# Optimization experiments

Hardware: AMD Instinct MI355X
Metric: run time of the kernel (lower is better)

Reference implementation:

```python
import jax, jax.numpy as jnp
import numpy as np

B, N, C, H, T = 64, 4096, 768, 12, 10


def setup_inputs() -> dict:
    key = jax.random.key(0)
    kx, kq, kk, kv, kp = jax.random.split(key, 5)
    std = 0.02  # trunc_normal std from _init_weights
    return {
        "x": jax.random.normal(kx, (B, N, C), jnp.float32),
        "Wq": std * jax.random.normal(kq, (C, C), jnp.float32),
        "Wk": std * jax.random.normal(kk, (C, C), jnp.float32),
        "Wv": std * jax.random.normal(kv, (C, C), jnp.float32),
        "Wp": std * jax.random.normal(kp, (C, C), jnp.float32),
        "bp": jnp.zeros((C,), jnp.float32),
        "nb_task_tokens": T,
    }


def reference(x, Wq, Wk, Wv, Wp, bp, nb_task_tokens):
    Bq, Nq, Cq = x.shape
    d = Cq // H
    scale = d ** -0.5
    Tt = nb_task_tokens
    # q only from the first T (task) tokens; k, v from all N tokens
    q = (x[:, :Tt] @ Wq).reshape(Bq, Tt, H, d).transpose(0, 2, 1, 3) * scale  # [B,H,T,d]
    k = (x @ Wk).reshape(Bq, Nq, H, d).transpose(0, 2, 1, 3)                  # [B,H,N,d]
    v = (x @ Wv).reshape(Bq, Nq, H, d).transpose(0, 2, 1, 3)                  # [B,H,N,d]
    attn = jnp.einsum("bhtd,bhnd->bhtn", q, k)                                # [B,H,T,N]
    # mask: task token i may attend to itself and to all patch tokens (cols >= T),
    # but not to other task tokens
    rows = jnp.arange(Tt)[:, None]
    cols = jnp.arange(Nq)[None, :]
    allowed = (cols >= Tt) | (cols == rows)                                   # [T,N]
    attn = jnp.where(allowed, attn, -jnp.inf)
    attn = jax.nn.softmax(attn, axis=-1)
    x_cls = jnp.einsum("bhtn,bhnd->bhtd", attn, v)                            # [B,H,T,d]
    x_cls = x_cls.transpose(0, 2, 1, 3).reshape(Bq, Tt, Cq)
    x_cls = x_cls @ Wp + bp
    return (x_cls, attn, v)
```

## Files before the change

kernel.cpp:

```cpp
#include <hip/hip_runtime.h>

typedef __attribute__((ext_vector_type(8))) short short8;
typedef __attribute__((ext_vector_type(4))) short short4v;
typedef __attribute__((ext_vector_type(4))) float f32x4;

__device__ __forceinline__ unsigned short f2bf(float f) {
  union { float f; unsigned u; } v; v.f = f;
  unsigned r = v.u + 0x7FFFu + ((v.u >> 16) & 1u);
  return (unsigned short)(r >> 16);
}

__device__ __forceinline__ void gload16(const void* g, void* l) {
  __builtin_amdgcn_global_load_lds(
      (const __attribute__((address_space(1))) void*)g,
      (__attribute__((address_space(3))) void*)l, 16, 0, 0);
}

__global__ __launch_bounds__(256) void conv_x(const float* __restrict__ x,
                                              unsigned short* __restrict__ xb) {
  const long total = 25165824;
  long stride = (long)gridDim.x * 256;
  for (long u = blockIdx.x * 256 + threadIdx.x; u < total; u += stride) {
    const float* p = x + u * 8;
    float4 a = *(const float4*)p;
    float4 b = *(const float4*)(p + 4);
    short8 h;
    h[0] = (short)f2bf(a.x); h[1] = (short)f2bf(a.y);
    h[2] = (short)f2bf(a.z); h[3] = (short)f2bf(a.w);
    h[4] = (short)f2bf(b.x); h[5] = (short)f2bf(b.y);
    h[6] = (short)f2bf(b.z); h[7] = (short)f2bf(b.w);
    *(short8*)(xb + u * 8) = h;
  }
}

__global__ __launch_bounds__(256) void prep_w(const float* __restrict__ Wk,
                                              const float* __restrict__ Wv,
                                              unsigned short* __restrict__ Wt) {
  int idx = blockIdx.x * 256 + threadIdx.x;
  int n = idx / 768, k = idx - n * 768;
  float w = (n < 768) ? Wk[k * 768 + n] : Wv[k * 768 + (n - 768)];
  Wt[idx] = f2bf(w);
}

__global__ __launch_bounds__(256) void q_proj(const float* __restrict__ x,
                                              const float* __restrict__ Wq,
                                              unsigned short* __restrict__ q_ws) {
  int b = blockIdx.x, tid = threadIdx.x;
  __shared__ float xr[7680];
  const float* xp = x + (long)b * 4096 * 768;
  for (int i = tid; i < 7680; i += 256) xr[i] = xp[i];
  for (int i = tid; i < 12 * 6 * 64; i += 256) {
    int h = i / 384, rem = i - h * 384;
    int t = 10 + rem / 64, d = rem & 63;
    q_ws[(((long)(b * 12 + h) * 16 + t) << 6) + d] = 0;
  }
  __syncthreads();
  float acc[10][3];
#pragma unroll
  for (int t = 0; t < 10; ++t) { acc[t][0] = 0.f; acc[t][1] = 0.f; acc[t][2] = 0.f; }
  for (int k = 0; k < 768; ++k) {
    const float* wr = Wq + (long)k * 768;
    float w0 = wr[tid], w1 = wr[tid + 256], w2 = wr[tid + 512];
#pragma unroll
    for (int t = 0; t < 10; ++t) {
      float xv = xr[t * 768 + k];
      acc[t][0] += xv * w0; acc[t][1] += xv * w1; acc[t][2] += xv * w2;
    }
  }
#pragma unroll
  for (int t = 0; t < 10; ++t) {
#pragma unroll
    for (int j = 0; j < 3; ++j) {
      int c = tid + j * 256;
      int h = c >> 6, d = c & 63;
      q_ws[(((long)(b * 12 + h) * 16 + t) << 6) + d] = f2bf(acc[t][j] * 0.125f);
    }
  }
}

__global__ __launch_bounds__(256) void gemm_kv5(const unsigned short* __restrict__ xb,
                                                const unsigned short* __restrict__ Wt,
                                                unsigned short* __restrict__ k_ws,
                                                float* __restrict__ v_out) {
  __shared__ char smem[49152];
#define A0 ((unsigned short*)(smem + 0))
#define B0 ((unsigned short*)(smem + 8192))
#define A1 ((unsigned short*)(smem + 16384))
#define B1 ((unsigned short*)(smem + 24576))
#define A2 ((unsigned short*)(smem + 32768))
#define B2 ((unsigned short*)(smem + 40960))

  int bid = blockIdx.x;
  int lb = (bid & 7) * 3072 + (bid >> 3);
  int mt = lb / 12, nt = lb - mt * 12;
  long m0 = (long)mt * 128; int n0 = nt * 128;
  int tid = threadIdx.x, lane = tid & 63;
  int uw = __builtin_amdgcn_readfirstlane(tid >> 6);
  int wm = uw >> 1, wn = uw & 1;
  int r16 = lane & 15, gk = lane >> 4;

  const unsigned short* xs = xb + m0 * 768;
  const unsigned short* wp = Wt + (long)n0 * 768;

  int srow = lane >> 2;
  int sg = ((lane & 3) ^ ((srow >> 1) & 3)) << 3;
  int sw = (gk ^ ((r16 >> 1) & 3)) << 3;

  int c0 = uw, c1 = uw + 4;
  const unsigned short* pA0 = xs + (long)(c0 * 16 + srow) * 768 + sg;
  const unsigned short* pA1 = xs + (long)(c1 * 16 + srow) * 768 + sg;
  const unsigned short* pB0 = wp + (long)(c0 * 16 + srow) * 768 + sg;
  const unsigned short* pB1 = wp + (long)(c1 * 16 + srow) * 768 + sg;

  f32x4 acc[4][4];
#pragma unroll
  for (int i = 0; i < 4; ++i)
#pragma unroll
    for (int j = 0; j < 4; ++j) acc[i][j] = (f32x4){0.f, 0.f, 0.f, 0.f};

#define STAGE(Ab, Bb, OFF)                                                      \
  {                                                                             \
    gload16(pA0 + (OFF), &Ab[c0 * 512]);                                        \
    gload16(pA1 + (OFF), &Ab[c1 * 512]);                                        \
    gload16(pB0 + (OFF), &Bb[c0 * 512]);                                        \
    gload16(pB1 + (OFF), &Bb[c1 * 512]);                                        \
  }
#define COMPUTE(Ab, Bb)                                                         \
  {                                                                             \
    short8 af[4], bfr[4];                                                       \
    _Pragma("unroll")                                                           \
    for (int mi = 0; mi < 4; ++mi)                                              \
      af[mi] = *(const short8*)&Ab[(wm * 64 + mi * 16 + r16) * 32 + sw];        \
    _Pragma("unroll")                                                           \
    for (int ni = 0; ni < 4; ++ni)                                              \
      bfr[ni] = *(const short8*)&Bb[(wn * 64 + ni * 16 + r16) * 32 + sw];       \
    _Pragma("unroll")                                                           \
    for (int mi = 0; mi < 4; ++mi)                                              \
      _Pragma("unroll")                                                         \
      for (int ni = 0; ni < 4; ++ni)                                            \
        acc[mi][ni] = __builtin_amdgcn_mfma_f32_16x16x32_bf16(af[mi], bfr[ni],  \
                                                              acc[mi][ni], 0, 0, 0); \
  }
#define WB4 asm volatile("s_waitcnt vmcnt(4) lgkmcnt(0)\n\ts_barrier" ::: "memory")
#define WB0 asm volatile("s_waitcnt vmcnt(0) lgkmcnt(0)\n\ts_barrier" ::: "memory")

  STAGE(A0, B0, 0);
  STAGE(A1, B1, 32);
  WB4;

#pragma unroll 1
  for (int g = 0; g < 7; ++g) {
    STAGE(A2, B2, 64);  COMPUTE(A0, B0); WB4;
    STAGE(A0, B0, 96);  COMPUTE(A1, B1); WB4;
    STAGE(A1, B1, 128); COMPUTE(A2, B2); WB4;
    pA0 += 96; pA1 += 96; pB0 += 96; pB1 += 96;
  }
  STAGE(A2, B2, 64); COMPUTE(A0, B0); WB4;
  COMPUTE(A1, B1); WB0;
  COMPUTE(A2, B2);

#undef STAGE
#undef COMPUTE
#undef WB4
#undef WB0

  float* scr = (float*)(smem + uw * 4096);
  bool is_k = (n0 < 768);
  int cb = is_k ? n0 : n0 - 768;
  int hq = (cb >> 6) + wn;
  int b12h = 0;

#pragma unroll
  for (int mi = 0; mi < 4; ++mi) {
#pragma unroll
    for (int ni = 0; ni < 4; ++ni)
#pragma unroll
      for (int r = 0; r < 4; ++r)
        scr[(gk * 4 + r) * 64 + ni * 16 + r16] = acc[mi][ni][r];
    long mbase = m0 + wm * 64 + mi * 16;
    if (is_k) {
#pragma unroll
      for (int p = 0; p < 2; ++p) {
        int row = p * 8 + (lane >> 3), d0 = (lane & 7) << 3;
        long m = mbase + row;
        int b = (int)(m >> 12), n = (int)(m & 4095);
        float4 aa = *(const float4*)&scr[row * 64 + d0];
        float4 bb = *(const float4*)&scr[row * 64 + d0 + 4];
        short8 hh;
        hh[0] = (short)f2bf(aa.x); hh[1] = (short)f2bf(aa.y);
        hh[2] = (short)f2bf(aa.z); hh[3] = (short)f2bf(aa.w);
        hh[4] = (short)f2bf(bb.x); hh[5] = (short)f2bf(bb.y);
        hh[6] = (short)f2bf(bb.z); hh[7] = (short)f2bf(bb.w);
        *(short8*)&k_ws[((long)(b * 12 + hq) * 4096 + n) * 64 + d0] = hh;
      }
    } else {
#pragma unroll
      for (int p = 0; p < 4; ++p) {
        int row = p * 4 + (lane >> 4), d0 = (lane & 15) << 2;
        long m = mbase + row;
        int b = (int)(m >> 12), n = (int)(m & 4095);
        float4 aa = *(const float4*)&scr[row * 64 + d0];
        *(float4*)&v_out[((long)(b * 12 + hq) * 4096 + n) * 64 + d0] = aa;
      }
    }
  }
  (void)b12h;
#undef A0
#undef B0
#undef A1
#undef B1
#undef A2
#undef B2
}

__global__ __launch_bounds__(256) void gemm_kv(const float* __restrict__ x,
                                               const unsigned short* __restrict__ Wt,
                                               unsigned short* __restrict__ k_ws,
                                               float* __restrict__ v_out) {
  __shared__ char lds[32768];
  int bid = blockIdx.x;
  int lb = (bid & 7) * 3072 + (bid >> 3);
  int mt = lb / 12, nt = lb - mt * 12;
  long m0 = (long)mt * 128; int n0 = nt * 128;
  int tid = threadIdx.x, lane = tid & 63;
  int wid = tid >> 6, wm = wid >> 1, wn = wid & 1;
  int rlo = lane & 15, gk = lane >> 4;

  const float* xs = x + m0 * 768;
  const unsigned short* wp = Wt + (long)n0 * 768;

  int arow0 = tid >> 3, ak4 = (tid & 7) << 2;
  int bn = tid >> 1, bg = (tid & 1) << 1;

  f32x4 acc[4][4];
#pragma unroll
  for (int i = 0; i < 4; ++i)
#pragma unroll
    for (int j = 0; j < 4; ++j) acc[i][j] = (f32x4){0.f, 0.f, 0.f, 0.f};

  float4 fA[4]; short8 wB[2];
#pragma unroll
  for (int it = 0; it < 4; ++it) {
    int row = it * 32 + arow0;
    fA[it] = *(const float4*)(xs + (long)row * 768 + ak4);
  }
#pragma unroll
  for (int i = 0; i < 2; ++i)
    wB[i] = *(const short8*)(wp + (long)bn * 768 + (bg + i) * 8);
#pragma unroll
  for (int it = 0; it < 4; ++it) {
    int row = it * 32 + arow0;
    short4v h;
    h[0] = (short)f2bf(fA[it].x); h[1] = (short)f2bf(fA[it].y);
    h[2] = (short)f2bf(fA[it].z); h[3] = (short)f2bf(fA[it].w);
    *(short4v*)(lds + row * 64 + ((ak4 * 2) ^ (((row >> 1) & 3) << 4))) = h;
  }
#pragma unroll
  for (int i = 0; i < 2; ++i)
    *(short8*)(lds + 16384 + bn * 64 + (((bg + i) * 16) ^ (((bn >> 1) & 3) << 4))) = wB[i];
  __syncthreads();

#pragma unroll 2
  for (int ks = 0; ks < 24; ++ks) {
    char* Ab = lds + (ks & 1) * 8192;
    char* Bb = lds + 16384 + (ks & 1) * 8192;
    bool pf = (ks + 1 < 24);
    if (pf) {
#pragma unroll
      for (int it = 0; it < 4; ++it) {
        int row = it * 32 + arow0;
        fA[it] = *(const float4*)(xs + (long)row * 768 + (ks + 1) * 32 + ak4);
      }
#pragma unroll
      for (int i = 0; i < 2; ++i)
        wB[i] = *(const short8*)(wp + (long)bn * 768 + (ks + 1) * 32 + (bg + i) * 8);
    }
    short8 af[4], bfr[4];
#pragma unroll
    for (int mi = 0; mi < 4; ++mi) {
      int row = wm * 64 + mi * 16 + rlo;
      af[mi] = *(const short8*)(Ab + row * 64 + ((gk * 16) ^ (((row >> 1) & 3) << 4)));
    }
#pragma unroll
    for (int ni = 0; ni < 4; ++ni) {
      int n = wn * 64 + ni * 16 + rlo;
      bfr[ni] = *(const short8*)(Bb + n * 64 + ((gk * 16) ^ (((n >> 1) & 3) << 4)));
    }
#pragma unroll
    for (int mi = 0; mi < 4; ++mi)
#pragma unroll
      for (int ni = 0; ni < 4; ++ni)
        acc[mi][ni] = __builtin_amdgcn_mfma_f32_16x16x32_bf16(af[mi], bfr[ni], acc[mi][ni], 0, 0, 0);
    if (pf) {
      char* An = lds + ((ks + 1) & 1) * 8192;
      char* Bn = lds + 16384 + ((ks + 1) & 1) * 8192;
#pragma unroll
      for (int it = 0; it < 4; ++it) {
        int row = it * 32 + arow0;
        short4v h;
        h[0] = (short)f2bf(fA[it].x); h[1] = (short)f2bf(fA[it].y);
        h[2] = (short)f2bf(fA[it].z); h[3] = (short)f2bf(fA[it].w);
        *(short4v*)(An + row * 64 + ((ak4 * 2) ^ (((row >> 1) & 3) << 4))) = h;
      }
#pragma unroll
      for (int i = 0; i < 2; ++i)
        *(short8*)(Bn + bn * 64 + (((bg + i) * 16) ^ (((bn >> 1) & 3) << 4))) = wB[i];
    }
    __syncthreads();
  }

  bool is_k = (n0 < 768);
  int cb = is_k ? n0 : n0 - 768;
#pragma unroll
  for (int ni = 0; ni < 4; ++ni) {
    int cc = cb + wn * 64 + ni * 16 + rlo;
    int h = cc >> 6, d = cc & 63;
#pragma unroll
    for (int mi = 0; mi < 4; ++mi) {
#pragma unroll
      for (int r = 0; r < 4; ++r) {
        long m = m0 + wm * 64 + mi * 16 + gk * 4 + r;
        int b = (int)(m >> 12), n = (int)(m & 4095);
        long off = ((long)(b * 12 + h) * 4096 + n) * 64 + d;
        float val = acc[mi][ni][r];
        if (is_k) k_ws[off] = f2bf(val);
        else      v_out[off] = val;
      }
    }
  }
}

__global__ __launch_bounds__(512) void attn_fused(const unsigned short* __restrict__ k_ws,
                                                  const unsigned short* __restrict__ q_ws,
                                                  const float* __restrict__ v_glob,
                                                  float* __restrict__ attn_out,
                                                  float* __restrict__ preproj) {
  __shared__ float red[8][16];
  __shared__ float rowmax[16];
  __shared__ float rowinv[16];
  __shared__ float scratch[8 * 256];

  int tid = threadIdx.x, lane = tid & 63, w = tid >> 6;
  int bh = blockIdx.x;
  int r16 = lane & 15, gk = lane >> 4;
  int trc = (r16 < 10) ? r16 : 9;

  const unsigned short* kp = k_ws + (long)bh * (4096 * 64);
  const unsigned short* qp = q_ws + (long)bh * 1024;
  float* sraw = attn_out + (long)bh * 40960;
  const float* vp = v_glob + (long)bh * (4096 * 64);

  short8 qf0 = *(const short8*)(qp + r16 * 64 + gk * 8);
  short8 qf1 = *(const short8*)(qp + r16 * 64 + 32 + gk * 8);

  float pmax = -3.0e38f;
  for (int ch = 0; ch < 32; ++ch) {
    int n0 = (w * 32 + ch) << 4;
    short8 kf0 = *(const short8*)(kp + (long)(n0 + r16) * 64 + gk * 8);
    short8 kf1 = *(const short8*)(kp + (long)(n0 + r16) * 64 + 32 + gk * 8);
    f32x4 d4 = (f32x4){0.f, 0.f, 0.f, 0.f};
    d4 = __builtin_amdgcn_mfma_f32_16x16x32_bf16(kf0, qf0, d4, 0, 0, 0);
    d4 = __builtin_amdgcn_mfma_f32_16x16x32_bf16(kf1, qf1, d4, 0, 0, 0);
    float sv[4];
#pragma unroll
    for (int r = 0; r < 4; ++r) {
      int n = n0 + gk * 4 + r;
      float s = d4[r];
      if (n < 10 && n != r16) s = -1e30f;
      sv[r] = s;
      pmax = fmaxf(pmax, s);
    }
    if (r16 < 10)
      *(float4*)(sraw + r16 * 4096 + n0 + gk * 4) = make_float4(sv[0], sv[1], sv[2], sv[3]);
  }
  pmax = fmaxf(pmax, __shfl_xor(pmax, 16));
  pmax = fmaxf(pmax, __shfl_xor(pmax, 32));
  if (lane < 16) red[w][lane] = pmax;
  __syncthreads();
  if (tid < 16) {
    float m = red[0][tid];
#pragma unroll
    for (int i = 1; i < 8; ++i) m = fmaxf(m, red[i][tid]);
    rowmax[tid] = m;
  }
  __syncthreads();

  float mx = rowmax[trc];
  float psum = 0.f;
  for (int ch = 0; ch < 16; ++ch) {
    int n0 = ((w * 16 + ch) << 5) + gk * 8;
    float4 a = *(const float4*)(sraw + trc * 4096 + n0);
    float4 b2 = *(const float4*)(sraw + trc * 4096 + n0 + 4);
    psum += __expf(a.x - mx) + __expf(a.y - mx) + __expf(a.z - mx) + __expf(a.w - mx)
          + __expf(b2.x - mx) + __expf(b2.y - mx) + __expf(b2.z - mx) + __expf(b2.w - mx);
  }
  psum += __shfl_xor(psum, 16);
  psum += __shfl_xor(psum, 32);
  if (lane < 16) red[w][lane] = psum;
  __syncthreads();
  if (tid < 16) {
    float s = 0.f;
#pragma unroll
    for (int i = 0; i < 8; ++i) s += red[i][tid];
    rowinv[tid] = 1.0f / s;
  }
  __syncthreads();

  int dc = w & 3, half = w >> 2;
  int d0 = dc << 4;
  float inv = rowinv[trc];
  f32x4 acc = (f32x4){0.f, 0.f, 0.f, 0.f};
  for (int kk = 0; kk < 64; ++kk) {
    int nr = half * 2048 + kk * 32 + gk * 8;
    float* sp = sraw + trc * 4096 + nr;
    float4 s0 = *(const float4*)(sp);
    float4 s1 = *(const float4*)(sp + 4);
    float p0 = __expf(s0.x - mx) * inv, p1 = __expf(s0.y - mx) * inv;
    float p2 = __expf(s0.z - mx) * inv, p3 = __expf(s0.w - mx) * inv;
    float p4 = __expf(s1.x - mx) * inv, p5 = __expf(s1.y - mx) * inv;
    float p6 = __expf(s1.z - mx) * inv, p7 = __expf(s1.w - mx) * inv;
    if (r16 < 10) {
      *(float4*)(sp)     = make_float4(p0, p1, p2, p3);
      *(float4*)(sp + 4) = make_float4(p4, p5, p6, p7);
    }
    short8 pa;
    pa[0] = (short)f2bf(p0); pa[1] = (short)f2bf(p1);
    pa[2] = (short)f2bf(p2); pa[3] = (short)f2bf(p3);
    pa[4] = (short)f2bf(p4); pa[5] = (short)f2bf(p5);
    pa[6] = (short)f2bf(p6); pa[7] = (short)f2bf(p7);
    short8 vb;
    const float* vrow = vp + (long)nr * 64 + d0 + r16;
#pragma unroll
    for (int j = 0; j < 8; ++j) vb[j] = (short)f2bf(vrow[j * 64]);
    acc = __builtin_amdgcn_mfma_f32_16x16x32_bf16(pa, vb, acc, 0, 0, 0);
  }
#pragma unroll
  for (int r = 0; r < 4; ++r)
    scratch[w * 256 + (gk * 4 + r) * 16 + r16] = acc[r];
  __syncthreads();

  int b = bh / 12, h = bh - b * 12;
  for (int idx = tid; idx < 640; idx += 512) {
    int tt = idx >> 6, d = idx & 63;
    int c = d >> 4, dl = d & 15;
    float s = scratch[c * 256 + tt * 16 + dl] + scratch[(c + 4) * 256 + tt * 16 + dl];
    preproj[((long)b * 10 + tt) * 768 + h * 64 + d] = s;
  }
}

__global__ __launch_bounds__(256) void proj_out_k(const float* __restrict__ preproj,
                                                  const float* __restrict__ Wp,
                                                  const float* __restrict__ bp,
                                                  float* __restrict__ out0) {
  int b = blockIdx.x, tid = threadIdx.x;
  __shared__ float xr[7680];
  const float* pp = preproj + (long)b * 7680;
  for (int i = tid; i < 7680; i += 256) xr[i] = pp[i];
  __syncthreads();
  float acc[10][3];
#pragma unroll
  for (int t = 0; t < 10; ++t) { acc[t][0] = 0.f; acc[t][1] = 0.f; acc[t][2] = 0.f; }
  for (int k = 0; k < 768; ++k) {
    const float* wr = Wp + (long)k * 768;
    float w0 = wr[tid], w1 = wr[tid + 256], w2 = wr[tid + 512];
#pragma unroll
    for (int t = 0; t < 10; ++t) {
      float xv = xr[t * 768 + k];
      acc[t][0] += xv * w0; acc[t][1] += xv * w1; acc[t][2] += xv * w2;
    }
  }
  float b0 = bp[tid], b1 = bp[tid + 256], b2 = bp[tid + 512];
  float* op = out0 + (long)b * 7680;
#pragma unroll
  for (int t = 0; t < 10; ++t) {
    op[t * 768 + tid]       = acc[t][0] + b0;
    op[t * 768 + tid + 256] = acc[t][1] + b1;
    op[t * 768 + tid + 512] = acc[t][2] + b2;
  }
}

extern "C" void kernel_launch(void* const* d_in, const int* in_sizes, int n_in,
                              void* d_out, int out_size, void* d_ws, size_t ws_size,
                              hipStream_t stream) {
  (void)in_sizes; (void)n_in; (void)out_size;
  const float* x  = (const float*)d_in[0];
  const float* Wq = (const float*)d_in[1];
  const float* Wk = (const float*)d_in[2];
  const float* Wv = (const float*)d_in[3];
  const float* Wp = (const float*)d_in[4];
  const float* bp = (const float*)d_in[5];

  float* out      = (float*)d_out;
  float* attn_out = out + 491520;
  float* v_out    = out + 31948800;

  char* ws = (char*)d_ws;
  const size_t NEED_BIG = 811204608;

  if (ws_size >= NEED_BIG) {
    unsigned short* x_bf16 = (unsigned short*)(ws);
    unsigned short* k_ws = (unsigned short*)(ws + 402653184);
    unsigned short* q_ws = (unsigned short*)(ws + 805306368);
    unsigned short* Wt   = (unsigned short*)(ws + 806879232);
    float* preproj       = (float*)(ws + 809238528);

    conv_x<<<dim3(2048), dim3(256), 0, stream>>>(x, x_bf16);
    prep_w<<<dim3(4608), dim3(256), 0, stream>>>(Wk, Wv, Wt);
    q_proj<<<dim3(64), dim3(256), 0, stream>>>(x, Wq, q_ws);
    gemm_kv5<<<dim3(24576), dim3(256), 0, stream>>>(x_bf16, Wt, k_ws, v_out);
    attn_fused<<<dim3(768), dim3(512), 0, stream>>>(k_ws, q_ws, v_out, attn_out, preproj);
    proj_out_k<<<dim3(64), dim3(256), 0, stream>>>(preproj, Wp, bp, out);
  } else {
    unsigned short* k_ws = (unsigned short*)(ws);
    unsigned short* q_ws = (unsigned short*)(ws + 402653184);
    unsigned short* Wt   = (unsigned short*)(ws + 404226048);
    float* preproj       = (float*)(ws + 406585344);

    prep_w<<<dim3(4608), dim3(256), 0, stream>>>(Wk, Wv, Wt);
    q_proj<<<dim3(64), dim3(256), 0, stream>>>(x, Wq, q_ws);
    gemm_kv<<<dim3(24576), dim3(256), 0, stream>>>(x, Wt, k_ws, v_out);
    attn_fused<<<dim3(768), dim3(512), 0, stream>>>(k_ws, q_ws, v_out, attn_out, preproj);
    proj_out_k<<<dim3(64), dim3(256), 0, stream>>>(preproj, Wp, bp, out);
  }
}
```

Measured before the change: 1.775 ms.

## Enlarge KV GEMM tile to 256x256 with 8 waves per block

Replaces the 128x128 KV-projection GEMM kernel with a 256x256-tile version using 512 threads (8 waves, each computing 128x64), doubling LDS buffers to 96KB with a triple-buffered K pipeline. The goal is to raise arithmetic intensity and cut redundant global/L2 loads of x and W per output element. The LDS swizzle is simplified and the epilogue scratch uses a padded stride of 68 to avoid bank conflicts. The tradeoffs are higher register pressure (32 accumulators per wave) and lower occupancy from the 96KB of LDS per block.

```diff
diff --git a/kernel.cpp b/kernel.cpp
--- a/kernel.cpp
+++ b/kernel.cpp
@@ -78,64 +78,59 @@
   }
 }
 
-__global__ __launch_bounds__(256) void gemm_kv5(const unsigned short* __restrict__ xb,
-                                                const unsigned short* __restrict__ Wt,
-                                                unsigned short* __restrict__ k_ws,
-                                                float* __restrict__ v_out) {
-  __shared__ char smem[49152];
-#define A0 ((unsigned short*)(smem + 0))
-#define B0 ((unsigned short*)(smem + 8192))
-#define A1 ((unsigned short*)(smem + 16384))
-#define B1 ((unsigned short*)(smem + 24576))
-#define A2 ((unsigned short*)(smem + 32768))
-#define B2 ((unsigned short*)(smem + 40960))
+__global__ __launch_bounds__(512, 2) void gemm_kv6(const unsigned short* __restrict__ xb,
+                                                   const unsigned short* __restrict__ Wt,
+                                                   unsigned short* __restrict__ k_ws,
+                                                   float* __restrict__ v_out) {
+  __shared__ char smem[98304];
+#define AB(i) ((unsigned short*)(smem + (i) * 16384))
 
   int bid = blockIdx.x;
-  int lb = (bid & 7) * 3072 + (bid >> 3);
-  int mt = lb / 12, nt = lb - mt * 12;
-  long m0 = (long)mt * 128; int n0 = nt * 128;
+  int lb = (bid & 7) * 768 + (bid >> 3);
+  int mt = lb / 6, nt = lb - mt * 6;
+  long m0 = (long)mt * 256; int n0 = nt * 256;
   int tid = threadIdx.x, lane = tid & 63;
   int uw = __builtin_amdgcn_readfirstlane(tid >> 6);
-  int wm = uw >> 1, wn = uw & 1;
+  int wm = uw >> 2, wn = uw & 3;
   int r16 = lane & 15, gk = lane >> 4;
 
   const unsigned short* xs = xb + m0 * 768;
   const unsigned short* wp = Wt + (long)n0 * 768;
 
   int srow = lane >> 2;
-  int sg = ((lane & 3) ^ ((srow >> 1) & 3)) << 3;
-  int sw = (gk ^ ((r16 >> 1) & 3)) << 3;
-
-  int c0 = uw, c1 = uw + 4;
-  const unsigned short* pA0 = xs + (long)(c0 * 16 + srow) * 768 + sg;
-  const unsigned short* pA1 = xs + (long)(c1 * 16 + srow) * 768 + sg;
-  const unsigned short* pB0 = wp + (long)(c0 * 16 + srow) * 768 + sg;
-  const unsigned short* pB1 = wp + (long)(c1 * 16 + srow) * 768 + sg;
-
-  f32x4 acc[4][4];
-#pragma unroll
-  for (int i = 0; i < 4; ++i)
+  int schunk = ((lane & 3) ^ (srow & 3)) << 3;
+  const unsigned short* pA = xs + (long)(uw * 16 + srow) * 768 + schunk;
+  const unsigned short* pB = wp + (long)(uw * 16 + srow) * 768 + schunk;
+  const long JROW = 128 * 768;
+
+  int rc = (gk ^ (r16 & 3)) << 3;
+
+  f32x4 acc[8][4];
+#pragma unroll
+  for (int i = 0; i < 8; ++i)
 #pragma unroll
     for (int j = 0; j < 4; ++j) acc[i][j] = (f32x4){0.f, 0.f, 0.f, 0.f};
 
-#define STAGE(Ab, Bb, OFF)                                                      \
+#define STAGE(BUF, OFF)                                                         \
   {                                                                             \
-    gload16(pA0 + (OFF), &Ab[c0 * 512]);                                        \
-    gload16(pA1 + (OFF), &Ab[c1 * 512]);                                        \
-    gload16(pB0 + (OFF), &Bb[c0 * 512]);                                        \
-    gload16(pB1 + (OFF), &Bb[c1 * 512]);                                        \
-  }
-#define COMPUTE(Ab, Bb)                                                         \
+    gload16(pA + (OFF), AB(2 * (BUF)) + uw * 512);                              \
+    gload16(pA + (OFF) + JROW, AB(2 * (BUF)) + uw * 512 + 4096);                \
+    gload16(pB + (OFF), AB(2 * (BUF) + 1) + uw * 512);                          \
+    gload16(pB + (OFF) + JROW, AB(2 * (BUF) + 1) + uw * 512 + 4096);            \
+  }
+#define COMPUTE(BUF)                                                            \
   {                                                                             \
-    short8 af[4], bfr[4];                                                       \
+    const unsigned short* Ab = AB(2 * (BUF));                                   \
+    const unsigned short* Bb = AB(2 * (BUF) + 1);                               \
+    short8 af[8], bfr[4];                                                       \
     _Pragma("unroll")                                                           \
-    for (int mi = 0; mi < 4; ++mi)                                              \
-      af[mi] = *(const short8*)&Ab[(wm * 64 + mi * 16 + r16) * 32 + sw];        \
+    for (int mi = 0; mi < 8; ++mi)                                              \
+      af[mi] = *(const short8*)&Ab[(wm * 128 + mi * 16 + r16) * 32 + rc];       \
     _Pragma("unroll")                                                           \
     for (int ni = 0; ni < 4; ++ni)                                              \
-      bfr[ni] = *(const short8*)&Bb[(wn * 64 + ni * 16 + r16) * 32 + sw];       \
+      bfr[ni] = *(const short8*)&Bb[(wn * 64 + ni * 16 + r16) * 32 + rc];       \
     _Pragma("unroll")                                                           \
-    for (int mi = 0; mi < 4; ++mi)                                              \
+    for (int mi = 0; mi < 8; ++mi)                                              \
       _Pragma("unroll")                                                         \
       for (int ni = 0; ni < 4; ++ni)                                            \
         acc[mi][ni] = __builtin_amdgcn_mfma_f32_16x16x32_bf16(af[mi], bfr[ni],  \
@@ -144,73 +139,63 @@
 #define WB4 asm volatile("s_waitcnt vmcnt(4) lgkmcnt(0)\n\ts_barrier" ::: "memory")
 #define WB0 asm volatile("s_waitcnt vmcnt(0) lgkmcnt(0)\n\ts_barrier" ::: "memory")
 
-  STAGE(A0, B0, 0);
-  STAGE(A1, B1, 32);
+  STAGE(0, 0);
+  STAGE(1, 32);
   WB4;
 
 #pragma unroll 1
   for (int g = 0; g < 7; ++g) {
-    STAGE(A2, B2, 64);  COMPUTE(A0, B0); WB4;
-    STAGE(A0, B0, 96);  COMPUTE(A1, B1); WB4;
-    STAGE(A1, B1, 128); COMPUTE(A2, B2); WB4;
-    pA0 += 96; pA1 += 96; pB0 += 96; pB1 += 96;
-  }
-  STAGE(A2, B2, 64); COMPUTE(A0, B0); WB4;
-  COMPUTE(A1, B1); WB0;
-  COMPUTE(A2, B2);
+    STAGE(2, 64);  COMPUTE(0); WB4;
+    STAGE(0, 96);  COMPUTE(1); WB4;
+    STAGE(1, 128); COMPUTE(2); WB4;
+    pA += 96; pB += 96;
+  }
+  STAGE(2, 64); COMPUTE(0); WB4;
+  COMPUTE(1); WB0;
+  COMPUTE(2);
 
 #undef STAGE
 #undef COMPUTE
 #undef WB4
 #undef WB0
 
-  float* scr = (float*)(smem + uw * 4096);
+  float* scr = (float*)smem + uw * 1088;
   bool is_k = (n0 < 768);
-  int cb = is_k ? n0 : n0 - 768;
-  int hq = (cb >> 6) + wn;
-  int b12h = 0;
-
-#pragma unroll
-  for (int mi = 0; mi < 4; ++mi) {
+  int h = (is_k ? (n0 >> 6) : ((n0 - 768) >> 6)) + wn;
+  int bq = (int)(m0 >> 12);
+  int nb = (int)(m0 & 4095) + wm * 128;
+
+#pragma unroll
+  for (int mi = 0; mi < 8; ++mi) {
 #pragma unroll
     for (int ni = 0; ni < 4; ++ni)
 #pragma unroll
       for (int r = 0; r < 4; ++r)
-        scr[(gk * 4 + r) * 64 + ni * 16 + r16] = acc[mi][ni][r];
-    long mbase = m0 + wm * 64 + mi * 16;
+        scr[(gk * 4 + r) * 68 + ni * 16 + r16] = acc[mi][ni][r];
+    int nbase = nb + mi * 16;
     if (is_k) {
 #pragma unroll
       for (int p = 0; p < 2; ++p) {
         int row = p * 8 + (lane >> 3), d0 = (lane & 7) << 3;
-        long m = mbase + row;
-        int b = (int)(m >> 12), n = (int)(m & 4095);
-        float4 aa = *(const float4*)&scr[row * 64 + d0];
-        float4 bb = *(const float4*)&scr[row * 64 + d0 + 4];
+        float4 aa = *(const float4*)&scr[row * 68 + d0];
+        float4 bb = *(const float4*)&scr[row * 68 + d0 + 4];
         short8 hh;
         hh[0] = (short)f2bf(aa.x); hh[1] = (short)f2bf(aa.y);
         hh[2] = (short)f2bf(aa.z); hh[3] = (short)f2bf(aa.w);
         hh[4] = (short)f2bf(bb.x); hh[5] = (short)f2bf(bb.y);
         hh[6] = (short)f2bf(bb.z); hh[7] = (short)f2bf(bb.w);
-        *(short8*)&k_ws[((long)(b * 12 + hq) * 4096 + n) * 64 + d0] = hh;
+        *(short8*)&k_ws[((long)(bq * 12 + h) * 4096 + nbase + row) * 64 + d0] = hh;
       }
     } else {
 #pragma unroll
       for (int p = 0; p < 4; ++p) {
         int row = p * 4 + (lane >> 4), d0 = (lane & 15) << 2;
-        long m = mbase + row;
-        int b = (int)(m >> 12), n = (int)(m & 4095);
-        float4 aa = *(const float4*)&scr[row * 64 + d0];
-        *(float4*)&v_out[((long)(b * 12 + hq) * 4096 + n) * 64 + d0] = aa;
+        float4 aa = *(const float4*)&scr[row * 68 + d0];
+        *(float4*)&v_out[((long)(bq * 12 + h) * 4096 + nbase + row) * 64 + d0] = aa;
       }
     }
   }
-  (void)b12h;
-#undef A0
-#undef B0
-#undef A1
-#undef B1
-#undef A2
-#undef B2
+#undef AB
 }
 
 __global__ __launch_bounds__(256) void gemm_kv(const float* __restrict__ x,
@@ -507,7 +492,7 @@
     conv_x<<<dim3(2048), dim3(256), 0, stream>>>(x, x_bf16);
     prep_w<<<dim3(4608), dim3(256), 0, stream>>>(Wk, Wv, Wt);
     q_proj<<<dim3(64), dim3(256), 0, stream>>>(x, Wq, q_ws);
-    gemm_kv5<<<dim3(24576), dim3(256), 0, stream>>>(x_bf16, Wt, k_ws, v_out);
+    gemm_kv6<<<dim3(6144), dim3(512), 0, stream>>>(x_bf16, Wt, k_ws, v_out);
     attn_fused<<<dim3(768), dim3(512), 0, stream>>>(k_ws, q_ws, v_out, attn_out, preproj);
     proj_out_k<<<dim3(64), dim3(256), 0, stream>>>(preproj, Wp, bp, out);
   } else {
```

After: 1.628 ms. 1.09x faster.
